# Kernel tuning notes

Hardware: AMD Instinct MI355X
Metric: run time of the kernel (lower is better)

Reference implementation:

```python
import jax, jax.numpy as jnp
import numpy as np

N_NODES = 50000
N_EDGES = 800000
IN_CH = 128
OUT_CH = 64
HEADS = 2
NEG_SLOPE = 0.2


def _gat_conv(x, src, dst, W, a_src, a_dst, b, n):
    """PyG-style GATConv (eval mode: no dropout), self-loops already appended.
    x: [n, F_in]; W: [F_in, H*C]; a_src/a_dst: [H, C]; b: [H*C]."""
    H, C = a_src.shape
    h = (x @ W).reshape(n, H, C)                       # [n, H, C]
    alpha_src = jnp.sum(h * a_src, axis=-1)            # [n, H]
    alpha_dst = jnp.sum(h * a_dst, axis=-1)            # [n, H]
    e = alpha_src[src] + alpha_dst[dst]                # [E, H]
    e = jnp.where(e > 0, e, NEG_SLOPE * e)             # LeakyReLU(0.2)
    # neighbor-wise (destination-grouped) softmax, numerically stable
    m = jax.ops.segment_max(e, dst, num_segments=n)
    e = jnp.exp(e - m[dst])
    denom = jax.ops.segment_sum(e, dst, num_segments=n)
    alpha = e / (denom[dst] + 1e-16)                   # [E, H]
    out = jax.ops.segment_sum(alpha[:, :, None] * h[src], dst, num_segments=n)
    return out.reshape(n, H * C) + b


def setup_inputs() -> dict:
    key = jax.random.key(0)
    ks = jax.random.split(key, 12)
    s = 0.08  # glorot-ish scale
    x = jax.random.normal(ks[0], (N_NODES, IN_CH), dtype=jnp.float32)
    edge_index = jax.random.randint(ks[1], (2, N_EDGES), 0, N_NODES, dtype=jnp.int64)
    H, O = HEADS, OUT_CH
    return {
        "x": x,
        "edge_index": edge_index,
        "W1": jax.random.normal(ks[2], (IN_CH, H * 2 * O), dtype=jnp.float32) * s,
        "a_src1": jax.random.normal(ks[3], (H, 2 * O), dtype=jnp.float32) * s,
        "a_dst1": jax.random.normal(ks[4], (H, 2 * O), dtype=jnp.float32) * s,
        "b1": jnp.zeros((H * 2 * O,), dtype=jnp.float32),
        "W_mu": jax.random.normal(ks[5], (2 * O * H, H * O), dtype=jnp.float32) * s,
        "a_src_mu": jax.random.normal(ks[6], (H, O), dtype=jnp.float32) * s,
        "a_dst_mu": jax.random.normal(ks[7], (H, O), dtype=jnp.float32) * s,
        "b_mu": jnp.zeros((H * O,), dtype=jnp.float32),
        "W_ls": jax.random.normal(ks[8], (2 * O * H, H * O), dtype=jnp.float32) * s,
        "a_src_ls": jax.random.normal(ks[9], (H, O), dtype=jnp.float32) * s,
        "a_dst_ls": jax.random.normal(ks[10], (H, O), dtype=jnp.float32) * s,
        "b_ls": jnp.zeros((H * O,), dtype=jnp.float32),
    }


def reference(x, edge_index, W1, a_src1, a_dst1, b1,
              W_mu, a_src_mu, a_dst_mu, b_mu,
              W_ls, a_src_ls, a_dst_ls, b_ls):
    n = x.shape[0]
    loop = jnp.arange(n, dtype=edge_index.dtype)
    src = jnp.concatenate([edge_index[0], loop])  # PyG add_self_loops=True
    dst = jnp.concatenate([edge_index[1], loop])
    x1 = jax.nn.elu(_gat_conv(x, src, dst, W1, a_src1, a_dst1, b1, n))
    mu = _gat_conv(x1, src, dst, W_mu, a_src_mu, a_dst_mu, b_mu, n)
    logstd = _gat_conv(x1, src, dst, W_ls, a_src_ls, a_dst_ls, b_ls, n)
    return (mu, logstd)
```

## Files before the change

### kernel.cpp

```cpp
#include <hip/hip_runtime.h>


typedef unsigned short u16;
typedef unsigned int u32;
typedef _Float16 f16;
typedef f16 f16x8 __attribute__((ext_vector_type(8)));
typedef float f32x4v __attribute__((ext_vector_type(4)));

__device__ __forceinline__ u16 f2h(float f) {
    union { f16 h; u16 u; } t;
    t.h = (f16)f;
    return t.u;
}
__device__ __forceinline__ float4 loadh4(const u16* __restrict__ p, size_t i) {
    union { uint2 u; f16 h[4]; } t;
    t.u = *(const uint2*)(p + i);
    return make_float4((float)t.h[0], (float)t.h[1], (float)t.h[2], (float)t.h[3]);
}
__device__ __forceinline__ void store4(float* __restrict__ p, size_t i, float4 v) {
    *(float4*)(p + i) = v;
}
__device__ __forceinline__ void store4(u16* __restrict__ p, size_t i, float4 v) {
    union { uint2 u; f16 h[4]; } t;
    t.h[0] = (f16)v.x; t.h[1] = (f16)v.y; t.h[2] = (f16)v.z; t.h[3] = (f16)v.w;
    *(uint2*)(p + i) = t.u;
}

__global__ __launch_bounds__(256) void k_detect(const u32* __restrict__ ebuf,
                                                int* __restrict__ flag) {
    __shared__ int nz;
    if (threadIdx.x == 0) nz = 0;
    __syncthreads();
    if (ebuf[2 * threadIdx.x + 1] != 0u) atomicAdd(&nz, 1);
    __syncthreads();
    if (threadIdx.x == 0) *flag = (nz == 0) ? 1 : 0;
}

__global__ __launch_bounds__(256) void k_extract(const u32* __restrict__ ebuf, int E,
                                                 const int* __restrict__ flag,
                                                 int* __restrict__ se,
                                                 int* __restrict__ de,
                                                 int* __restrict__ deg) {
    int e = blockIdx.x * 256 + threadIdx.x;
    if (e >= E) return;
    int s, d;
    if (*flag) {
        s = (int)ebuf[2 * (size_t)e];
        d = (int)ebuf[2 * ((size_t)E + (size_t)e)];
    } else {
        s = (int)ebuf[e];
        d = (int)ebuf[(size_t)E + (size_t)e];
    }
    se[e] = s;
    de[e] = d;
    atomicAdd(&deg[d], 1);
}

__global__ __launch_bounds__(256) void k_scan_a(const int* __restrict__ deg, int n,
                                                int* __restrict__ bsum) {
    __shared__ int s[256];
    int i = blockIdx.x * 256 + threadIdx.x;
    s[threadIdx.x] = (i < n) ? deg[i] : 0;
    __syncthreads();
    for (int st = 128; st > 0; st >>= 1) {
        if (threadIdx.x < st) s[threadIdx.x] += s[threadIdx.x + st];
        __syncthreads();
    }
    if (threadIdx.x == 0) bsum[blockIdx.x] = s[0];
}

__global__ __launch_bounds__(256) void k_scan_b(int* __restrict__ bsum, int nb) {
    __shared__ int s[256];
    int t = threadIdx.x;
    int v = (t < nb) ? bsum[t] : 0;
    s[t] = v;
    __syncthreads();
    for (int off = 1; off < 256; off <<= 1) {
        int add = (t >= off) ? s[t - off] : 0;
        __syncthreads();
        s[t] += add;
        __syncthreads();
    }
    if (t < nb) bsum[t] = s[t] - v;
}

__global__ __launch_bounds__(256) void k_scan_c(const int* __restrict__ deg, int n,
                                                const int* __restrict__ bsum,
                                                int* __restrict__ rowptr,
                                                int* __restrict__ cursor, int E) {
    __shared__ int s[256];
    int t = threadIdx.x;
    int i = blockIdx.x * 256 + t;
    int v = (i < n) ? deg[i] : 0;
    s[t] = v;
    __syncthreads();
    for (int off = 1; off < 256; off <<= 1) {
        int add = (t >= off) ? s[t - off] : 0;
        __syncthreads();
        s[t] += add;
        __syncthreads();
    }
    if (i < n) {
        int ex = bsum[blockIdx.x] + s[t] - v;
        rowptr[i] = ex;
        cursor[i] = ex;
    }
    if (i == 0) rowptr[n] = E;
}

__global__ __launch_bounds__(256) void k_fill(const int* __restrict__ src,
                                              const int* __restrict__ dst, int E,
                                              int* __restrict__ cursor,
                                              int* __restrict__ csr_src) {
    int e = blockIdx.x * 256 + threadIdx.x;
    if (e < E) {
        int d = dst[e];
        int slot = atomicAdd(&cursor[d], 1);
        csr_src[slot] = src[e];
    }
}

__global__ __launch_bounds__(256) void k_cvt(const float* __restrict__ in,
                                             u16* __restrict__ out, int nElem) {
    int i = (blockIdx.x * 256 + threadIdx.x) * 4;
    if (i >= nElem) return;
    float4 v = *(const float4*)(in + i);
    store4(out, i, v);
}

__global__ __launch_bounds__(256) void k_tw(const float* __restrict__ Wl,
                                            const float* __restrict__ Wr, int split,
                                            int K, u16* __restrict__ Wt) {
    int idx = blockIdx.x * 256 + threadIdx.x;
    if (idx >= 256 * K) return;
    int c = idx / K, k = idx - c * K;
    float v;
    if (split == 256)
        v = Wl[(size_t)k * 256 + c];
    else
        v = (c < 128) ? Wl[(size_t)k * 128 + c] : Wr[(size_t)k * 128 + (c - 128)];
    Wt[idx] = f2h(v);
}

template <int K, int ALOGW>
__global__ __launch_bounds__(256) void k_gemm_mfma(
    const u16* __restrict__ Ah, const u16* __restrict__ Wt, u16* __restrict__ out,
    float* __restrict__ as_out, float* __restrict__ ad_out,
    const float* __restrict__ alo, const float* __restrict__ ahi,
    const float* __restrict__ dlo, const float* __restrict__ dhi, int M) {
    __shared__ u16 Bs[256 * 40];
    const int tid = threadIdx.x;
    const int wave = tid >> 6;
    const int lane = tid & 63;
    const int li = lane & 15;
    const int quad = lane >> 4;
    const int r0 = blockIdx.x * 64 + wave * 16;
    int arowi = r0 + li;
    if (arowi >= M) arowi = M - 1;
    const u16* arow = Ah + (size_t)arowi * K + quad * 8;

    f32x4v acc[16];
#pragma unroll
    for (int ct = 0; ct < 16; ct++) acc[ct] = (f32x4v)(0.f);

    for (int t = 0; t < K; t += 32) {
        __syncthreads();
        {
            const u16* src = Wt + (size_t)tid * K + t;
            u16* dst = Bs + tid * 40;
            uint4 v0 = ((const uint4*)src)[0];
            uint4 v1 = ((const uint4*)src)[1];
            uint4 v2 = ((const uint4*)src)[2];
            uint4 v3 = ((const uint4*)src)[3];
            ((uint4*)dst)[0] = v0;
            ((uint4*)(dst + 8))[0] = v1;
            ((uint4*)(dst + 16))[0] = v2;
            ((uint4*)(dst + 24))[0] = v3;
        }
        __syncthreads();
        f16x8 a = *(const f16x8*)(arow + t);
#pragma unroll
        for (int ct = 0; ct < 16; ct++) {
            f16x8 b = *(const f16x8*)(Bs + (ct * 16 + li) * 40 + quad * 8);
            acc[ct] = __builtin_amdgcn_mfma_f32_16x16x32_f16(a, b, acc[ct], 0, 0, 0);
        }
    }

#pragma unroll
    for (int reg = 0; reg < 4; reg++) {
        int grow = r0 + quad * 4 + reg;
        if (grow < M) {
            u16* orow = out + (size_t)grow * 256 + li;
#pragma unroll
            for (int ct = 0; ct < 16; ct++) orow[ct * 16] = f2h(acc[ct][reg]);
        }
    }

    const int NS = 64 >> ALOGW;
    const int SH = ALOGW - 2;
    float aw[16], dw[16];
#pragma unroll
    for (int ct = 0; ct < 16; ct++) {
        int col = ct * 16 + li;
        aw[ct] = (col < 128) ? alo[col] : ahi[col - 128];
        dw[ct] = (col < 128) ? dlo[col] : dhi[col - 128];
    }
#pragma unroll
    for (int reg = 0; reg < 4; reg++) {
        float s[4] = {0.f, 0.f, 0.f, 0.f};
        float d[4] = {0.f, 0.f, 0.f, 0.f};
#pragma unroll
        for (int ct = 0; ct < 16; ct++) {
            int sl = ct >> SH;
            s[sl] += acc[ct][reg] * aw[ct];
            d[sl] += acc[ct][reg] * dw[ct];
        }
#pragma unroll
        for (int sl = 0; sl < NS; sl++) {
#pragma unroll
            for (int m = 1; m <= 8; m <<= 1) {
                s[sl] += __shfl_xor(s[sl], m, 64);
                d[sl] += __shfl_xor(d[sl], m, 64);
            }
        }
        int grow = r0 + quad * 4 + reg;
        if (li == 0 && grow < M) {
#pragma unroll
            for (int sl = 0; sl < NS; sl++) {
                as_out[(size_t)grow * NS + sl] = s[sl];
                ad_out[(size_t)grow * NS + sl] = d[sl];
            }
        }
    }
}

template <int LOGW, int MODE, typename OT>
__global__ __launch_bounds__(256) void k_agg(const u16* __restrict__ h,
                                             const int* __restrict__ rowptr,
                                             const int* __restrict__ csr_src,
                                             const float* __restrict__ as,
                                             const float* __restrict__ ad,
                                             const float* __restrict__ b_lo,
                                             const float* __restrict__ b_hi,
                                             OT* __restrict__ outp, int n) {
    const int NS = 64 >> LOGW;
    int wid = blockIdx.x * 4 + (threadIdx.x >> 6);
    int lane = threadIdx.x & 63;
    if (wid >= n) return;
    int slot = lane >> LOGW;
    int c = lane * 4;

    float adv = ad[(size_t)wid * NS + slot];
    float e = as[(size_t)wid * NS + slot] + adv;
    e = fmaxf(e, 0.2f * e);
    float w = __expf(e);
    float denom = w;
    float4 hv = loadh4(h, (size_t)wid * 256 + c);
    float acc0 = w * hv.x, acc1 = w * hv.y, acc2 = w * hv.z, acc3 = w * hv.w;

    const int rb = rowptr[wid], re = rowptr[wid + 1];
    int p = rb;
    for (; p + 4 <= re; p += 4) {
        int s0 = csr_src[p], s1 = csr_src[p + 1];
        int s2 = csr_src[p + 2], s3 = csr_src[p + 3];
        float e0 = as[(size_t)s0 * NS + slot] + adv;
        float e1 = as[(size_t)s1 * NS + slot] + adv;
        float e2 = as[(size_t)s2 * NS + slot] + adv;
        float e3 = as[(size_t)s3 * NS + slot] + adv;
        e0 = fmaxf(e0, 0.2f * e0);
        e1 = fmaxf(e1, 0.2f * e1);
        e2 = fmaxf(e2, 0.2f * e2);
        e3 = fmaxf(e3, 0.2f * e3);
        float w0 = __expf(e0), w1 = __expf(e1), w2 = __expf(e2), w3 = __expf(e3);
        float4 h0 = loadh4(h, (size_t)s0 * 256 + c);
        float4 h1 = loadh4(h, (size_t)s1 * 256 + c);
        float4 h2 = loadh4(h, (size_t)s2 * 256 + c);
        float4 h3 = loadh4(h, (size_t)s3 * 256 + c);
        denom += (w0 + w1) + (w2 + w3);
        acc0 += w0 * h0.x + w1 * h1.x + w2 * h2.x + w3 * h3.x;
        acc1 += w0 * h0.y + w1 * h1.y + w2 * h2.y + w3 * h3.y;
        acc2 += w0 * h0.z + w1 * h1.z + w2 * h2.z + w3 * h3.z;
        acc3 += w0 * h0.w + w1 * h1.w + w2 * h2.w + w3 * h3.w;
    }
    for (; p < re; ++p) {
        int s = csr_src[p];
        float ev = as[(size_t)s * NS + slot] + adv;
        ev = fmaxf(ev, 0.2f * ev);
        float ww = __expf(ev);
        denom += ww;
        float4 hh = loadh4(h, (size_t)s * 256 + c);
        acc0 += ww * hh.x;
        acc1 += ww * hh.y;
        acc2 += ww * hh.z;
        acc3 += ww * hh.w;
    }
    float inv = 1.0f / (denom + 1e-16f);

    int ci = c & 127;
    const float* bp = (c < 128) ? b_lo : b_hi;
    float4 bv = *(const float4*)(bp + ci);
    float v0 = acc0 * inv + bv.x;
    float v1 = acc1 * inv + bv.y;
    float v2 = acc2 * inv + bv.z;
    float v3 = acc3 * inv + bv.w;

    if (MODE == 0) {
        v0 = v0 > 0.f ? v0 : expm1f(v0);
        v1 = v1 > 0.f ? v1 : expm1f(v1);
        v2 = v2 > 0.f ? v2 : expm1f(v2);
        v3 = v3 > 0.f ? v3 : expm1f(v3);
        store4(outp, (size_t)wid * 256 + c, make_float4(v0, v1, v2, v3));
    } else {
        size_t base = (c < 128) ? ((size_t)wid * 128 + c)
                                : ((size_t)n * 128 + (size_t)wid * 128 + (c - 128));
        store4(outp, base, make_float4(v0, v1, v2, v3));
    }
}

extern "C" void kernel_launch(void* const* d_in, const int* in_sizes, int n_in,
                              void* d_out, int out_size, void* d_ws, size_t ws_size,
                              hipStream_t stream) {
    const float* x = (const float*)d_in[0];
    const u32* ebuf = (const u32*)d_in[1];
    const float* W1 = (const float*)d_in[2];
    const float* a_src1 = (const float*)d_in[3];
    const float* a_dst1 = (const float*)d_in[4];
    const float* b1 = (const float*)d_in[5];
    const float* W_mu = (const float*)d_in[6];
    const float* a_src_mu = (const float*)d_in[7];
    const float* a_dst_mu = (const float*)d_in[8];
    const float* b_mu = (const float*)d_in[9];
    const float* W_ls = (const float*)d_in[10];
    const float* a_src_ls = (const float*)d_in[11];
    const float* a_dst_ls = (const float*)d_in[12];
    const float* b_ls = (const float*)d_in[13];

    const int n = in_sizes[0] / 128;
    const int E = in_sizes[1] / 2;

    char* base = (char*)d_ws;
    size_t off = 0;
    auto alloc = [&](size_t b) -> char* {
        char* p = base + off;
        off = (off + b + 255) & ~(size_t)255;
        return p;
    };
    int* rowptr = (int*)alloc((size_t)(n + 1) * 4);
    int* cursor = (int*)alloc((size_t)n * 4);
    int* csr = (int*)alloc((size_t)E * 4);
    int* bsum = (int*)alloc(256 * 4);
    int* eflag = (int*)alloc(256);
    int* se = (int*)alloc((size_t)E * 4);
    int* de = (int*)alloc((size_t)E * 4);
    float* as = (float*)alloc((size_t)n * 4 * 4);
    float* ad = (float*)alloc((size_t)n * 4 * 4);
    u16* W1t = (u16*)alloc(256 * 128 * 2);
    u16* Wt2 = (u16*)alloc(256 * 256 * 2);
    u16* x1h = (u16*)alloc((size_t)n * 256 * 2);
    u16* xh = x1h;
    u16* h = (u16*)alloc((size_t)n * 256 * 2);

    const int nb = (n + 255) / 256;
    const int eg = (E + 255) / 256;
    const int ng4 = (n + 3) / 4;
    const int gg = (n + 63) / 64;

    hipMemsetAsync(cursor, 0, (size_t)n * 4, stream);
    k_detect<<<1, 256, 0, stream>>>(ebuf, eflag);
    k_extract<<<eg, 256, 0, stream>>>(ebuf, E, eflag, se, de, cursor);
    k_scan_a<<<nb, 256, 0, stream>>>(cursor, n, bsum);
    k_scan_b<<<1, 256, 0, stream>>>(bsum, nb);
    k_scan_c<<<nb, 256, 0, stream>>>(cursor, n, bsum, rowptr, cursor, E);
    k_fill<<<eg, 256, 0, stream>>>(se, de, E, cursor, csr);

    k_cvt<<<(n * 128 / 4 + 255) / 256, 256, 0, stream>>>(x, xh, n * 128);
    k_tw<<<(256 * 128 + 255) / 256, 256, 0, stream>>>(W1, W1, 256, 128, W1t);
    k_tw<<<(256 * 256 + 255) / 256, 256, 0, stream>>>(W_mu, W_ls, 128, 256, Wt2);

    k_gemm_mfma<128, 5><<<gg, 256, 0, stream>>>(xh, W1t, h, as, ad, a_src1,
                                                a_src1 + 128, a_dst1, a_dst1 + 128,
                                                n);
    k_agg<5, 0, u16><<<ng4, 256, 0, stream>>>(h, rowptr, csr, as, ad, b1, b1 + 128,
                                              x1h, n);

    k_gemm_mfma<256, 4><<<gg, 256, 0, stream>>>(x1h, Wt2, h, as, ad, a_src_mu,
                                                a_src_ls, a_dst_mu, a_dst_ls, n);
    k_agg<4, 1, float><<<ng4, 256, 0, stream>>>(h, rowptr, csr, as, ad, b_mu, b_ls,
                                                (float*)d_out, n);
}
```

Before: 384.0 us.

## Fuse prep kernels, register-prefetch 2x-tiled GEMM, and batch edge weights in aggregation

```diff
diff --git a/kernel.cpp b/kernel.cpp
--- a/kernel.cpp
+++ b/kernel.cpp
@@ -12,7 +12,7 @@
     t.h = (f16)f;
     return t.u;
 }
-__device__ __forceinline__ float4 loadh4(const u16* __restrict__ p, size_t i) {
+__device__ __forceinline__ float4 loadh4(const u16* __restrict__ p, u32 i) {
     union { uint2 u; f16 h[4]; } t;
     t.u = *(const uint2*)(p + i);
     return make_float4((float)t.h[0], (float)t.h[1], (float)t.h[2], (float)t.h[3]);
@@ -120,30 +120,36 @@
     }
 }
 
-__global__ __launch_bounds__(256) void k_cvt(const float* __restrict__ in,
-                                             u16* __restrict__ out, int nElem) {
-    int i = (blockIdx.x * 256 + threadIdx.x) * 4;
-    if (i >= nElem) return;
-    float4 v = *(const float4*)(in + i);
-    store4(out, i, v);
-}
-
-__global__ __launch_bounds__(256) void k_tw(const float* __restrict__ Wl,
-                                            const float* __restrict__ Wr, int split,
-                                            int K, u16* __restrict__ Wt) {
-    int idx = blockIdx.x * 256 + threadIdx.x;
-    if (idx >= 256 * K) return;
-    int c = idx / K, k = idx - c * K;
-    float v;
-    if (split == 256)
-        v = Wl[(size_t)k * 256 + c];
-    else
-        v = (c < 128) ? Wl[(size_t)k * 128 + c] : Wr[(size_t)k * 128 + (c - 128)];
-    Wt[idx] = f2h(v);
+__global__ __launch_bounds__(256) void k_prep(const float* __restrict__ x,
+                                              u16* __restrict__ xh, int B0, int nx4,
+                                              const float* __restrict__ W1,
+                                              u16* __restrict__ W1t,
+                                              const float* __restrict__ Wmu,
+                                              const float* __restrict__ Wls,
+                                              u16* __restrict__ Wt2) {
+    int b = blockIdx.x;
+    int t = threadIdx.x;
+    if (b < B0) {
+        int g = b * 256 + t;
+        if (g < nx4) {
+            float4 v = *(const float4*)(x + (size_t)g * 4);
+            store4(xh, (size_t)g * 4, v);
+        }
+    } else if (b < B0 + 128) {
+        int idx = (b - B0) * 256 + t;
+        int c = idx >> 7, k = idx & 127;
+        W1t[idx] = f2h(W1[(size_t)k * 256 + c]);
+    } else {
+        int idx = (b - B0 - 128) * 256 + t;
+        int c = idx >> 8, k = idx & 255;
+        float v = (c < 128) ? Wmu[(size_t)k * 128 + c]
+                            : Wls[(size_t)k * 128 + (c - 128)];
+        Wt2[idx] = f2h(v);
+    }
 }
 
 template <int K, int ALOGW>
-__global__ __launch_bounds__(256) void k_gemm_mfma(
+__global__ __launch_bounds__(128, 2) void k_gemm_mfma(
     const u16* __restrict__ Ah, const u16* __restrict__ Wt, u16* __restrict__ out,
     float* __restrict__ as_out, float* __restrict__ ad_out,
     const float* __restrict__ alo, const float* __restrict__ ahi,
@@ -154,45 +160,72 @@
     const int lane = tid & 63;
     const int li = lane & 15;
     const int quad = lane >> 4;
-    const int r0 = blockIdx.x * 64 + wave * 16;
-    int arowi = r0 + li;
-    if (arowi >= M) arowi = M - 1;
-    const u16* arow = Ah + (size_t)arowi * K + quad * 8;
-
-    f32x4v acc[16];
-#pragma unroll
-    for (int ct = 0; ct < 16; ct++) acc[ct] = (f32x4v)(0.f);
+    const int r0 = blockIdx.x * 64 + wave * 32;
+
+    int ar0 = r0 + li;
+    if (ar0 >= M) ar0 = M - 1;
+    int ar1 = r0 + 16 + li;
+    if (ar1 >= M) ar1 = M - 1;
+    const u16* arow0 = Ah + (size_t)ar0 * K + quad * 8;
+    const u16* arow1 = Ah + (size_t)ar1 * K + quad * 8;
+
+    f32x4v acc[2][16];
+#pragma unroll
+    for (int mt = 0; mt < 2; mt++)
+#pragma unroll
+        for (int ct = 0; ct < 16; ct++) acc[mt][ct] = (f32x4v)(0.f);
+
+    const int c0 = tid, c1 = tid + 128;
+    uint4 br[2][4];
+#pragma unroll
+    for (int i = 0; i < 4; i++) {
+        br[0][i] = ((const uint4*)(Wt + (size_t)c0 * K))[i];
+        br[1][i] = ((const uint4*)(Wt + (size_t)c1 * K))[i];
+    }
+    f16x8 a0 = *(const f16x8*)(arow0);
+    f16x8 a1 = *(const f16x8*)(arow1);
 
     for (int t = 0; t < K; t += 32) {
         __syncthreads();
-        {
-            const u16* src = Wt + (size_t)tid * K + t;
-            u16* dst = Bs + tid * 40;
-            uint4 v0 = ((const uint4*)src)[0];
-            uint4 v1 = ((const uint4*)src)[1];
-            uint4 v2 = ((const uint4*)src)[2];
-            uint4 v3 = ((const uint4*)src)[3];
-            ((uint4*)dst)[0] = v0;
-            ((uint4*)(dst + 8))[0] = v1;
-            ((uint4*)(dst + 16))[0] = v2;
-            ((uint4*)(dst + 24))[0] = v3;
-        }
-        __syncthreads();
-        f16x8 a = *(const f16x8*)(arow + t);
+        ((uint4*)(Bs + c0 * 40))[0] = br[0][0];
+        ((uint4*)(Bs + c0 * 40 + 8))[0] = br[0][1];
+        ((uint4*)(Bs + c0 * 40 + 16))[0] = br[0][2];
+        ((uint4*)(Bs + c0 * 40 + 24))[0] = br[0][3];
+        ((uint4*)(Bs + c1 * 40))[0] = br[1][0];
+        ((uint4*)(Bs + c1 * 40 + 8))[0] = br[1][1];
+        ((uint4*)(Bs + c1 * 40 + 16))[0] = br[1][2];
+        ((uint4*)(Bs + c1 * 40 + 24))[0] = br[1][3];
+        __syncthreads();
+        f16x8 a0n, a1n;
+        if (t + 32 < K) {
+#pragma unroll
+            for (int i = 0; i < 4; i++) {
+                br[0][i] = ((const uint4*)(Wt + (size_t)c0 * K + t + 32))[i];
+                br[1][i] = ((const uint4*)(Wt + (size_t)c1 * K + t + 32))[i];
+            }
+            a0n = *(const f16x8*)(arow0 + t + 32);
+            a1n = *(const f16x8*)(arow1 + t + 32);
+        }
 #pragma unroll
         for (int ct = 0; ct < 16; ct++) {
             f16x8 b = *(const f16x8*)(Bs + (ct * 16 + li) * 40 + quad * 8);
-            acc[ct] = __builtin_amdgcn_mfma_f32_16x16x32_f16(a, b, acc[ct], 0, 0, 0);
-        }
-    }
-
-#pragma unroll
-    for (int reg = 0; reg < 4; reg++) {
-        int grow = r0 + quad * 4 + reg;
-        if (grow < M) {
-            u16* orow = out + (size_t)grow * 256 + li;
-#pragma unroll
-            for (int ct = 0; ct < 16; ct++) orow[ct * 16] = f2h(acc[ct][reg]);
+            acc[0][ct] = __builtin_amdgcn_mfma_f32_16x16x32_f16(a0, b, acc[0][ct], 0, 0, 0);
+            acc[1][ct] = __builtin_amdgcn_mfma_f32_16x16x32_f16(a1, b, acc[1][ct], 0, 0, 0);
+        }
+        a0 = a0n;
+        a1 = a1n;
+    }
+
+#pragma unroll
+    for (int mt = 0; mt < 2; mt++) {
+#pragma unroll
+        for (int reg = 0; reg < 4; reg++) {
+            int grow = r0 + mt * 16 + quad * 4 + reg;
+            if (grow < M) {
+                u16* orow = out + (size_t)grow * 256 + li;
+#pragma unroll
+                for (int ct = 0; ct < 16; ct++) orow[ct * 16] = f2h(acc[mt][ct][reg]);
+            }
         }
     }
 
@@ -206,29 +239,32 @@
         dw[ct] = (col < 128) ? dlo[col] : dhi[col - 128];
     }
 #pragma unroll
-    for (int reg = 0; reg < 4; reg++) {
-        float s[4] = {0.f, 0.f, 0.f, 0.f};
-        float d[4] = {0.f, 0.f, 0.f, 0.f};
-#pragma unroll
-        for (int ct = 0; ct < 16; ct++) {
-            int sl = ct >> SH;
-            s[sl] += acc[ct][reg] * aw[ct];
-            d[sl] += acc[ct][reg] * dw[ct];
-        }
-#pragma unroll
-        for (int sl = 0; sl < NS; sl++) {
-#pragma unroll
-            for (int m = 1; m <= 8; m <<= 1) {
-                s[sl] += __shfl_xor(s[sl], m, 64);
-                d[sl] += __shfl_xor(d[sl], m, 64);
+    for (int mt = 0; mt < 2; mt++) {
+#pragma unroll
+        for (int reg = 0; reg < 4; reg++) {
+            float s[4] = {0.f, 0.f, 0.f, 0.f};
+            float d[4] = {0.f, 0.f, 0.f, 0.f};
+#pragma unroll
+            for (int ct = 0; ct < 16; ct++) {
+                int sl = ct >> SH;
+                s[sl] += acc[mt][ct][reg] * aw[ct];
+                d[sl] += acc[mt][ct][reg] * dw[ct];
             }
-        }
-        int grow = r0 + quad * 4 + reg;
-        if (li == 0 && grow < M) {
 #pragma unroll
             for (int sl = 0; sl < NS; sl++) {
-                as_out[(size_t)grow * NS + sl] = s[sl];
-                ad_out[(size_t)grow * NS + sl] = d[sl];
+#pragma unroll
+                for (int m = 1; m <= 8; m <<= 1) {
+                    s[sl] += __shfl_xor(s[sl], m, 64);
+                    d[sl] += __shfl_xor(d[sl], m, 64);
+                }
+            }
+            int grow = r0 + mt * 16 + quad * 4 + reg;
+            if (li == 0 && grow < M) {
+#pragma unroll
+                for (int sl = 0; sl < NS; sl++) {
+                    as_out[(size_t)grow * NS + sl] = s[sl];
+                    ad_out[(size_t)grow * NS + sl] = d[sl];
+                }
             }
         }
     }
@@ -248,51 +284,65 @@
     int lane = threadIdx.x & 63;
     if (wid >= n) return;
     int slot = lane >> LOGW;
+    int wsl = (lane >> 3) & (NS - 1);
+    int i8 = lane & 7;
     int c = lane * 4;
 
-    float adv = ad[(size_t)wid * NS + slot];
-    float e = as[(size_t)wid * NS + slot] + adv;
+    float adv_own = ad[(u32)wid * NS + slot];
+    float adv_w = ad[(u32)wid * NS + wsl];
+
+    float e = as[(u32)wid * NS + slot] + adv_own;
     e = fmaxf(e, 0.2f * e);
     float w = __expf(e);
     float denom = w;
-    float4 hv = loadh4(h, (size_t)wid * 256 + c);
-    float acc0 = w * hv.x, acc1 = w * hv.y, acc2 = w * hv.z, acc3 = w * hv.w;
+    float acc0, acc1, acc2, acc3;
+    {
+        union { uint2 u; f16 hh[4]; } t;
+        t.u = *(const uint2*)(h + ((u32)wid << 8) + c);
+        acc0 = w * (float)t.hh[0];
+        acc1 = w * (float)t.hh[1];
+        acc2 = w * (float)t.hh[2];
+        acc3 = w * (float)t.hh[3];
+    }
 
     const int rb = rowptr[wid], re = rowptr[wid + 1];
     int p = rb;
-    for (; p + 4 <= re; p += 4) {
-        int s0 = csr_src[p], s1 = csr_src[p + 1];
-        int s2 = csr_src[p + 2], s3 = csr_src[p + 3];
-        float e0 = as[(size_t)s0 * NS + slot] + adv;
-        float e1 = as[(size_t)s1 * NS + slot] + adv;
-        float e2 = as[(size_t)s2 * NS + slot] + adv;
-        float e3 = as[(size_t)s3 * NS + slot] + adv;
-        e0 = fmaxf(e0, 0.2f * e0);
-        e1 = fmaxf(e1, 0.2f * e1);
-        e2 = fmaxf(e2, 0.2f * e2);
-        e3 = fmaxf(e3, 0.2f * e3);
-        float w0 = __expf(e0), w1 = __expf(e1), w2 = __expf(e2), w3 = __expf(e3);
-        float4 h0 = loadh4(h, (size_t)s0 * 256 + c);
-        float4 h1 = loadh4(h, (size_t)s1 * 256 + c);
-        float4 h2 = loadh4(h, (size_t)s2 * 256 + c);
-        float4 h3 = loadh4(h, (size_t)s3 * 256 + c);
-        denom += (w0 + w1) + (w2 + w3);
-        acc0 += w0 * h0.x + w1 * h1.x + w2 * h2.x + w3 * h3.x;
-        acc1 += w0 * h0.y + w1 * h1.y + w2 * h2.y + w3 * h3.y;
-        acc2 += w0 * h0.z + w1 * h1.z + w2 * h2.z + w3 * h3.z;
-        acc3 += w0 * h0.w + w1 * h1.w + w2 * h2.w + w3 * h3.w;
+    for (; p + 8 <= re; p += 8) {
+        int sval = csr_src[p + i8];
+        float ee = as[(u32)sval * NS + wsl] + adv_w;
+        ee = fmaxf(ee, 0.2f * ee);
+        float wv = __expf(ee);
+        int si[8];
+        uint2 raw[8];
+#pragma unroll
+        for (int i = 0; i < 8; i++) si[i] = __shfl(sval, i, 64);
+#pragma unroll
+        for (int i = 0; i < 8; i++)
+            raw[i] = *(const uint2*)(h + ((u32)si[i] << 8) + c);
+#pragma unroll
+        for (int i = 0; i < 8; i++) {
+            float wi = __shfl(wv, slot * 8 + i, 64);
+            union { uint2 u; f16 hh[4]; } t;
+            t.u = raw[i];
+            denom += wi;
+            acc0 += wi * (float)t.hh[0];
+            acc1 += wi * (float)t.hh[1];
+            acc2 += wi * (float)t.hh[2];
+            acc3 += wi * (float)t.hh[3];
+        }
     }
     for (; p < re; ++p) {
         int s = csr_src[p];
-        float ev = as[(size_t)s * NS + slot] + adv;
+        float ev = as[(u32)s * NS + slot] + adv_own;
         ev = fmaxf(ev, 0.2f * ev);
         float ww = __expf(ev);
         denom += ww;
-        float4 hh = loadh4(h, (size_t)s * 256 + c);
-        acc0 += ww * hh.x;
-        acc1 += ww * hh.y;
-        acc2 += ww * hh.z;
-        acc3 += ww * hh.w;
+        union { uint2 u; f16 hh[4]; } t;
+        t.u = *(const uint2*)(h + ((u32)s << 8) + c);
+        acc0 += ww * (float)t.hh[0];
+        acc1 += ww * (float)t.hh[1];
+        acc2 += ww * (float)t.hh[2];
+        acc3 += ww * (float)t.hh[3];
     }
     float inv = 1.0f / (denom + 1e-16f);
 
@@ -364,6 +414,8 @@
     const int eg = (E + 255) / 256;
     const int ng4 = (n + 3) / 4;
     const int gg = (n + 63) / 64;
+    const int nx4 = n * 128 / 4;
+    const int B0 = (nx4 + 255) / 256;
 
     hipMemsetAsync(cursor, 0, (size_t)n * 4, stream);
     k_detect<<<1, 256, 0, stream>>>(ebuf, eflag);
@@ -373,17 +425,16 @@
     k_scan_c<<<nb, 256, 0, stream>>>(cursor, n, bsum, rowptr, cursor, E);
     k_fill<<<eg, 256, 0, stream>>>(se, de, E, cursor, csr);
 
-    k_cvt<<<(n * 128 / 4 + 255) / 256, 256, 0, stream>>>(x, xh, n * 128);
-    k_tw<<<(256 * 128 + 255) / 256, 256, 0, stream>>>(W1, W1, 256, 128, W1t);
-    k_tw<<<(256 * 256 + 255) / 256, 256, 0, stream>>>(W_mu, W_ls, 128, 256, Wt2);
-
-    k_gemm_mfma<128, 5><<<gg, 256, 0, stream>>>(xh, W1t, h, as, ad, a_src1,
+    k_prep<<<B0 + 128 + 256, 256, 0, stream>>>(x, xh, B0, nx4, W1, W1t, W_mu, W_ls,
+                                               Wt2);
+
+    k_gemm_mfma<128, 5><<<gg, 128, 0, stream>>>(xh, W1t, h, as, ad, a_src1,
                                                 a_src1 + 128, a_dst1, a_dst1 + 128,
                                                 n);
     k_agg<5, 0, u16><<<ng4, 256, 0, stream>>>(h, rowptr, csr, as, ad, b1, b1 + 128,
                                               x1h, n);
 
-    k_gemm_mfma<256, 4><<<gg, 256, 0, stream>>>(x1h, Wt2, h, as, ad, a_src_mu,
+    k_gemm_mfma<256, 4><<<gg, 128, 0, stream>>>(x1h, Wt2, h, as, ad, a_src_mu,
                                                 a_src_ls, a_dst_mu, a_dst_ls, n);
     k_agg<4, 1, float><<<ng4, 256, 0, stream>>>(h, rowptr, csr, as, ad, b_mu, b_ls,
                                                 (float*)d_out, n);
```

Result: slower. 419.4 us (+9.2%).
